# Kernel optimization log

Hardware: AMD Instinct MI355X
Metric: run time of the kernel (lower is better)

## Reference

```python
import jax, jax.numpy as jnp
import numpy as np

EMBED_DIM = 1024
NUM_HEADS = 16
HEAD_DIM = EMBED_DIM // NUM_HEADS


def setup_inputs() -> dict:
    key = jax.random.key(0)
    ks = jax.random.split(key, 11)
    B, S, E = 4, 2048, EMBED_DIM
    s = 1.0 / np.sqrt(E)
    return {
        "q": jax.random.normal(ks[0], (B, S, E), jnp.float32),
        "k": jax.random.normal(ks[1], (B, S, E), jnp.float32),
        "v": jax.random.normal(ks[2], (B, S, E), jnp.float32),
        "Wq": jax.random.uniform(ks[3], (E, E), jnp.float32, -s, s),
        "bq": jax.random.uniform(ks[4], (E,), jnp.float32, -s, s),
        "Wk": jax.random.uniform(ks[5], (E, E), jnp.float32, -s, s),
        "bk": jax.random.uniform(ks[6], (E,), jnp.float32, -s, s),
        "Wv": jax.random.uniform(ks[7], (E, E), jnp.float32, -s, s),
        "bv": jax.random.uniform(ks[8], (E,), jnp.float32, -s, s),
        "Wo": jax.random.uniform(ks[9], (E, E), jnp.float32, -s, s),
        "bo": jax.random.uniform(ks[10], (E,), jnp.float32, -s, s),
    }


def _split_heads(x):
    B, S, E = x.shape
    return x.reshape(B, S, NUM_HEADS, HEAD_DIM).transpose(0, 2, 1, 3)  # [B,H,S,D]


def reference(q, k, v, Wq, bq, Wk, bk, Wv, bv, Wo, bo):
    # torch Linear: x @ W.T + b
    Q = _split_heads(q @ Wq.T + bq)
    K = _split_heads(k @ Wk.T + bk)
    V = _split_heads(v @ Wv.T + bv)
    scale = 1.0 / jnp.sqrt(jnp.float32(HEAD_DIM))
    scores = jnp.einsum("bhqd,bhkd->bhqk", Q, K) * scale  # [B,H,S,S]
    weights = jax.nn.softmax(scores, axis=-1)
    ctx = jnp.einsum("bhqk,bhkd->bhqd", weights, V)
    B, H, S, D = ctx.shape
    merged = ctx.transpose(0, 2, 1, 3).reshape(B, S, H * D)
    out = merged @ Wo.T + bo
    return out, weights
```

## Files before the change

kernel.cpp:

```cpp
#include <hip/hip_runtime.h>
#include <hip/hip_bf16.h>

typedef __bf16 bf16x8 __attribute__((ext_vector_type(8)));
typedef float f32x4 __attribute__((ext_vector_type(4)));

constexpr size_t XQ_OFF = 0;
constexpr size_t WQ_OFF = 25165824;
constexpr size_t Q_OFF  = 29360128;
constexpr size_t KK_OFF = 37748736;
constexpr size_t VT_OFF = 46137344;
constexpr size_t CTX_OFF= 54525952;

__device__ __forceinline__ void gload16(const void* g, void* s) {
    __builtin_amdgcn_global_load_lds((__attribute__((address_space(1))) void*)g,
                                     (__attribute__((address_space(3))) void*)s, 16, 0, 0);
}
#define WAIT_VM0()   asm volatile("s_waitcnt vmcnt(0)" ::: "memory")
#define WAIT_VM4()   asm volatile("s_waitcnt vmcnt(4)" ::: "memory")
#define WAIT_LGKM0() asm volatile("s_waitcnt lgkmcnt(0)" ::: "memory")
#define BAR()        __builtin_amdgcn_s_barrier()

__global__ __launch_bounds__(256) void convert_k(
    const float* __restrict__ q, const float* __restrict__ k, const float* __restrict__ v,
    const float* __restrict__ Wq, const float* __restrict__ Wk, const float* __restrict__ Wv,
    const float* __restrict__ Wo, __bf16* __restrict__ ws) {
    int id = blockIdx.x * 256 + threadIdx.x;
    const int NX = 1048576;
    const int NW = 131072;
    const float* src; size_t dst; int local;
    if (id < 3 * NX) {
        int z = id / NX; local = id - z * NX;
        src = (z == 0) ? q : ((z == 1) ? k : v);
        dst = XQ_OFF + (size_t)z * 8388608;
    } else {
        int i2 = id - 3 * NX;
        int z = i2 / NW; local = i2 - z * NW;
        src = (z == 0) ? Wq : ((z == 1) ? Wk : ((z == 2) ? Wv : Wo));
        dst = WQ_OFF + (size_t)z * 1048576;
    }
    const float4* s4 = (const float4*)(src + (size_t)local * 8);
    float4 a = s4[0], b = s4[1];
    bf16x8 o;
    o[0]=(__bf16)a.x; o[1]=(__bf16)a.y; o[2]=(__bf16)a.z; o[3]=(__bf16)a.w;
    o[4]=(__bf16)b.x; o[5]=(__bf16)b.y; o[6]=(__bf16)b.z; o[7]=(__bf16)b.w;
    *(bf16x8*)(ws + dst + (size_t)local * 8) = o;
}

template<int MODE>
__global__ __launch_bounds__(256) void gemm_k(
    __bf16* __restrict__ ws,
    const float* __restrict__ bq, const float* __restrict__ bk,
    const float* __restrict__ bv, const float* __restrict__ bo,
    float* __restrict__ out) {
    const int K = 1024;
    unsigned n = blockIdx.x + 64u * (blockIdx.y + 8u * blockIdx.z);
    unsigned cpx = (MODE == 0) ? 192u : 64u;
    unsigned m_ = (n & 7u) * cpx + (n >> 3);
    unsigned bx = m_ & 63u;
    unsigned rest = m_ >> 6;
    unsigned by = rest & 7u;
    unsigned bz = rest >> 3;

    int z = (int)bz;
    const __bf16* A; const __bf16* Bm; const float* bias;
    if (MODE == 0) {
        A    = ws + XQ_OFF + (size_t)z * 8388608;
        Bm   = ws + WQ_OFF + (size_t)z * 1048576;
        bias = (z == 0) ? bq : ((z == 1) ? bk : bv);
    } else {
        A    = ws + CTX_OFF;
        Bm   = ws + WQ_OFF + (size_t)3 * 1048576;
        bias = bo;
    }
    int row0 = (int)bx * 128, col0 = (int)by * 128;
    __shared__ __align__(16) __bf16 As[2][128 * 32];
    __shared__ __align__(16) __bf16 Bs[2][128 * 32];
    int t = threadIdx.x, lane = t & 63, w = t >> 6;
    int wr = w >> 1, wc = w & 1;
    f32x4 acc[4][4];
#pragma unroll
    for (int i = 0; i < 4; ++i)
#pragma unroll
        for (int j = 0; j < 4; ++j) acc[i][j] = (f32x4){0.f, 0.f, 0.f, 0.f};

    auto stage = [&](int buf, int kt) {
#pragma unroll
        for (int i = 0; i < 2; ++i) {
            int e = ((i * 4 + w) * 64 + lane) * 8;
            int r = e >> 5, c = e & 31;
            gload16(A  + (size_t)(row0 + r) * K + kt + c, &As[buf][e]);
            gload16(Bm + (size_t)(col0 + r) * K + kt + c, &Bs[buf][e]);
        }
    };

    stage(0, 0);
    int cur = 0;
    for (int kt = 0; kt < K; kt += 32) {
        bool nx = kt + 32 < K;
        if (nx) { stage(cur ^ 1, kt + 32); WAIT_VM4(); }
        else    { WAIT_VM0(); }
        BAR();
        const __bf16* Ac = As[cur];
        const __bf16* Bc = Bs[cur];
        bf16x8 af[4], bfr[4];
#pragma unroll
        for (int f = 0; f < 4; ++f) {
            af[f]  = *(const bf16x8*)&Ac[(wr * 64 + f * 16 + (lane & 15)) * 32 + (lane >> 4) * 8];
            bfr[f] = *(const bf16x8*)&Bc[(wc * 64 + f * 16 + (lane & 15)) * 32 + (lane >> 4) * 8];
        }
#pragma unroll
        for (int fr = 0; fr < 4; ++fr)
#pragma unroll
            for (int fc = 0; fc < 4; ++fc)
                acc[fr][fc] = __builtin_amdgcn_mfma_f32_16x16x32_bf16(af[fr], bfr[fc], acc[fr][fc], 0, 0, 0);
        WAIT_LGKM0();
        BAR();
        cur ^= 1;
    }

    if (MODE == 0) {
        __bf16* dqk = ws + Q_OFF + (size_t)z * 8388608;
        __bf16* dvt = ws + VT_OFF;
#pragma unroll
        for (int fr = 0; fr < 4; ++fr)
#pragma unroll
            for (int fc = 0; fc < 4; ++fc)
#pragma unroll
                for (int r = 0; r < 4; ++r) {
                    int m = row0 + wr * 64 + fr * 16 + ((lane >> 4) << 2) + r;
                    int nn = col0 + wc * 64 + fc * 16 + (lane & 15);
                    float val = acc[fr][fc][r] + bias[nn];
                    int bb = m >> 11, s = m & 2047, h = nn >> 6, d = nn & 63;
                    size_t bh = (size_t)bb * 16 + h;
                    if (z < 2) dqk[bh * 131072 + (size_t)s * 64 + d] = (__bf16)val;
                    else       dvt[bh * 131072 + (size_t)d * 2048 + s] = (__bf16)val;
                }
    } else {
#pragma unroll
        for (int fr = 0; fr < 4; ++fr)
#pragma unroll
            for (int fc = 0; fc < 4; ++fc)
#pragma unroll
                for (int r = 0; r < 4; ++r) {
                    int m = row0 + wr * 64 + fr * 16 + ((lane >> 4) << 2) + r;
                    int nn = col0 + wc * 64 + fc * 16 + (lane & 15);
                    out[(size_t)m * 1024 + nn] = acc[fr][fc][r] + bias[nn];
                }
    }
}

__global__ __launch_bounds__(512) void attn_k(const __bf16* __restrict__ ws,
                                              __bf16* __restrict__ wsw,
                                              float* __restrict__ wout) {
    const __bf16* Qp  = ws + Q_OFF;
    const __bf16* Kp  = ws + KK_OFF;
    const __bf16* Vtp = ws + VT_OFF;
    __bf16* ctx = wsw + CTX_OFF;

    unsigned n = blockIdx.x + 16u * blockIdx.y;
    int bh = (int)((n & 7u) * 8u + ((n >> 3) >> 4));
    int q0 = (int)((n >> 3) & 15u) * 128;

    int t = threadIdx.x, lane = t & 63, w = t >> 6, g = lane >> 4;
    __shared__ __align__(16) __bf16 QP[128 * 64];
    __shared__ __align__(16) __bf16 Ks[2][64 * 64];
    __shared__ __align__(16) __bf16 Vts[2][64 * 64];
    const __bf16* Qb = Qp  + (size_t)bh * 131072;
    const __bf16* Kb = Kp  + (size_t)bh * 131072;
    const __bf16* Vb = Vtp + (size_t)bh * 131072;
    const float SCALE = 0.125f;

#pragma unroll
    for (int i = 0; i < 2; ++i) {
        int ch = t + 512 * i, r = ch >> 3, c8 = ch & 7;
        gload16(Qb + (size_t)(q0 + r) * 64 + ((c8 ^ (r & 7)) << 3), &QP[ch * 8]);
    }
    WAIT_VM0(); BAR();
    int qrow = w * 16 + (lane & 15);
    bf16x8 aq0 = *(const bf16x8*)((const char*)QP + qrow * 128 + ((g * 16) ^ ((qrow & 7) << 4)));
    bf16x8 aq1 = *(const bf16x8*)((const char*)QP + qrow * 128 + (((4 + g) * 16) ^ ((qrow & 7) << 4)));

    {
        int r = t >> 3, c8 = t & 7;
        gload16(Kb + (size_t)r * 64 + ((c8 ^ (r & 7)) << 3), &Ks[0][t * 8]);
    }
    WAIT_VM0(); BAR();
    float rs[4] = {0.f, 0.f, 0.f, 0.f};
    int cur = 0;
    for (int kt = 0; kt < 2048; kt += 64) {
        bool nx = kt < 1984;
        if (nx) {
            int r = t >> 3, c8 = t & 7;
            gload16(Kb + (size_t)(kt + 64 + r) * 64 + ((c8 ^ (r & 7)) << 3), &Ks[cur ^ 1][t * 8]);
        }
        const __bf16* Kc = Ks[cur];
#pragma unroll
        for (int kc = 0; kc < 4; ++kc) {
            int krow = kc * 16 + (lane & 15);
            bf16x8 b0 = *(const bf16x8*)((const char*)Kc + krow * 128 + ((g * 16) ^ ((krow & 7) << 4)));
            bf16x8 b1 = *(const bf16x8*)((const char*)Kc + krow * 128 + (((4 + g) * 16) ^ ((krow & 7) << 4)));
            f32x4 s = (f32x4){0.f, 0.f, 0.f, 0.f};
            s = __builtin_amdgcn_mfma_f32_16x16x32_bf16(aq0, b0, s, 0, 0, 0);
            s = __builtin_amdgcn_mfma_f32_16x16x32_bf16(aq1, b1, s, 0, 0, 0);
#pragma unroll
            for (int r4 = 0; r4 < 4; ++r4) rs[r4] += __expf(s[r4] * SCALE);
        }
        WAIT_LGKM0();
        if (nx) WAIT_VM0();
        BAR();
        cur ^= 1;
    }
#pragma unroll
    for (int m = 1; m < 16; m <<= 1)
#pragma unroll
        for (int r4 = 0; r4 < 4; ++r4) rs[r4] += __shfl_xor(rs[r4], m);
    float rinv[4];
#pragma unroll
    for (int r4 = 0; r4 < 4; ++r4) rinv[r4] = 1.f / rs[r4];

    {
        int r = t >> 3, c8 = t & 7;
        gload16(Kb + (size_t)r * 64   + ((c8 ^ (r & 7)) << 3), &Ks[0][t * 8]);
        gload16(Vb + (size_t)r * 2048 + ((c8 ^ (r & 7)) << 3), &Vts[0][t * 8]);
    }
    WAIT_VM0(); BAR();
    cur = 0;
    f32x4 cacc[4];
#pragma unroll
    for (int i = 0; i < 4; ++i) cacc[i] = (f32x4){0.f, 0.f, 0.f, 0.f};

    for (int kt = 0; kt < 2048; kt += 64) {
        bool nx = kt < 1984;
        if (nx) {
            int r = t >> 3, c8 = t & 7;
            gload16(Kb + (size_t)(kt + 64 + r) * 64 + ((c8 ^ (r & 7)) << 3), &Ks[cur ^ 1][t * 8]);
            gload16(Vb + (size_t)r * 2048 + (kt + 64) + ((c8 ^ (r & 7)) << 3), &Vts[cur ^ 1][t * 8]);
        }
        const __bf16* Kc = Ks[cur];
        const __bf16* Vc = Vts[cur];
#pragma unroll
        for (int kc = 0; kc < 4; ++kc) {
            int krow = kc * 16 + (lane & 15);
            bf16x8 b0 = *(const bf16x8*)((const char*)Kc + krow * 128 + ((g * 16) ^ ((krow & 7) << 4)));
            bf16x8 b1 = *(const bf16x8*)((const char*)Kc + krow * 128 + (((4 + g) * 16) ^ ((krow & 7) << 4)));
            f32x4 s = (f32x4){0.f, 0.f, 0.f, 0.f};
            s = __builtin_amdgcn_mfma_f32_16x16x32_bf16(aq0, b0, s, 0, 0, 0);
            s = __builtin_amdgcn_mfma_f32_16x16x32_bf16(aq1, b1, s, 0, 0, 0);
#pragma unroll
            for (int r4 = 0; r4 < 4; ++r4) {
                float e = __expf(s[r4] * SCALE) * rinv[r4];
                int prow = w * 16 + (g << 2) + r4;
                int pcol = kc * 16 + (lane & 15);
                *(__bf16*)((char*)QP + prow * 128 + ((pcol * 2) ^ ((prow & 7) << 4))) = (__bf16)e;
            }
        }
        WAIT_LGKM0();
        __builtin_amdgcn_sched_barrier(0);
        BAR();
#pragma unroll
        for (int i = 0; i < 2; ++i) {
            int ch = t + 512 * i, row = ch >> 3, c8 = ch & 7;
            bf16x8 p = *(const bf16x8*)((const char*)QP + row * 128 + ((c8 * 16) ^ ((row & 7) << 4)));
            f32x4 lo = (f32x4){(float)p[0], (float)p[1], (float)p[2], (float)p[3]};
            f32x4 hi = (f32x4){(float)p[4], (float)p[5], (float)p[6], (float)p[7]};
            float* dst = wout + ((size_t)bh * 2048 + q0 + row) * 2048 + kt + c8 * 8;
            *(f32x4*)dst = lo;
            *(f32x4*)(dst + 4) = hi;
        }
        int arow = w * 16 + (lane & 15);
#pragma unroll
        for (int ks = 0; ks < 2; ++ks) {
            bf16x8 ap = *(const bf16x8*)((const char*)QP + arow * 128 + ((ks * 64 + g * 16) ^ ((arow & 7) << 4)));
#pragma unroll
            for (int dc = 0; dc < 4; ++dc) {
                int vrow = dc * 16 + (lane & 15);
                bf16x8 bv = *(const bf16x8*)((const char*)Vc + vrow * 128 + ((ks * 64 + g * 16) ^ ((vrow & 7) << 4)));
                cacc[dc] = __builtin_amdgcn_mfma_f32_16x16x32_bf16(ap, bv, cacc[dc], 0, 0, 0);
            }
        }
        WAIT_LGKM0();
        if (nx) WAIT_VM0();
        BAR();
        cur ^= 1;
    }

    int bb = bh >> 4, h = bh & 15;
#pragma unroll
    for (int dc = 0; dc < 4; ++dc)
#pragma unroll
        for (int r4 = 0; r4 < 4; ++r4) {
            int qg = q0 + w * 16 + (g << 2) + r4;
            int d = dc * 16 + (lane & 15);
            ctx[((size_t)bb * 2048 + qg) * 1024 + h * 64 + d] = (__bf16)cacc[dc][r4];
        }
}

extern "C" void kernel_launch(void* const* d_in, const int* in_sizes, int n_in,
                              void* d_out, int out_size, void* d_ws, size_t ws_size,
                              hipStream_t stream) {
    const float* q  = (const float*)d_in[0];
    const float* k  = (const float*)d_in[1];
    const float* v  = (const float*)d_in[2];
    const float* Wq = (const float*)d_in[3];
    const float* bq = (const float*)d_in[4];
    const float* Wk = (const float*)d_in[5];
    const float* bk = (const float*)d_in[6];
    const float* Wv = (const float*)d_in[7];
    const float* bv = (const float*)d_in[8];
    const float* Wo = (const float*)d_in[9];
    const float* bo = (const float*)d_in[10];
    __bf16* ws = (__bf16*)d_ws;
    float* out  = (float*)d_out;
    float* wout = out + 8388608;

    convert_k<<<dim3(14336), dim3(256), 0, stream>>>(q, k, v, Wq, Wk, Wv, Wo, ws);
    gemm_k<0><<<dim3(64, 8, 3), dim3(256), 0, stream>>>(ws, bq, bk, bv, bo, out);
    attn_k<<<dim3(16, 64), dim3(512), 0, stream>>>(ws, ws, wout);
    gemm_k<1><<<dim3(64, 8, 1), dim3(256), 0, stream>>>(ws, bq, bk, bv, bo, out);
}
```

Before: 580.0 us.

## Split attention into rowsum and weights kernels with 256-row query tiles

The fused attention kernel is split into two launches. A rowsum kernel computes softmax denominators into workspace, and a weights/context kernel reads them. Each block now covers 256 query rows with two MFMA fragments per wave, which doubles reuse of each K/V tile loaded into LDS. The change also adds s_setprio around MFMA sections and relaxes the end-of-iteration wait to vmcnt(8) so weight-output stores need not drain. Costs are an extra launch, more LDS and registers per block, half as many blocks, and the rowsum buffer aliasing the start of the workspace where the converted q input sits (presumably dead by then).

```diff
diff --git a/kernel.cpp b/kernel.cpp
--- a/kernel.cpp
+++ b/kernel.cpp
@@ -17,6 +17,7 @@
 }
 #define WAIT_VM0()   asm volatile("s_waitcnt vmcnt(0)" ::: "memory")
 #define WAIT_VM4()   asm volatile("s_waitcnt vmcnt(4)" ::: "memory")
+#define WAIT_VM8()   asm volatile("s_waitcnt vmcnt(8)" ::: "memory")
 #define WAIT_LGKM0() asm volatile("s_waitcnt lgkmcnt(0)" ::: "memory")
 #define BAR()        __builtin_amdgcn_s_barrier()
 
@@ -149,43 +150,31 @@
     }
 }
 
-__global__ __launch_bounds__(512) void attn_k(const __bf16* __restrict__ ws,
-                                              __bf16* __restrict__ wsw,
-                                              float* __restrict__ wout) {
-    const __bf16* Qp  = ws + Q_OFF;
-    const __bf16* Kp  = ws + KK_OFF;
-    const __bf16* Vtp = ws + VT_OFF;
-    __bf16* ctx = wsw + CTX_OFF;
-
-    unsigned n = blockIdx.x + 16u * blockIdx.y;
-    int bh = (int)((n & 7u) * 8u + ((n >> 3) >> 4));
-    int q0 = (int)((n >> 3) & 15u) * 128;
-
+__global__ __launch_bounds__(512) void rowsum_k(const __bf16* __restrict__ ws,
+                                                float* __restrict__ rs_out) {
+    unsigned n = blockIdx.x + 8u * blockIdx.y;
+    unsigned m = (n & 7u) * 64u + (n >> 3);
+    int bh = (int)(m >> 3);
+    int q0 = (int)(m & 7u) * 256;
+    const __bf16* Qb = ws + Q_OFF  + (size_t)bh * 131072;
+    const __bf16* Kb = ws + KK_OFF + (size_t)bh * 131072;
+    __shared__ __align__(16) __bf16 Ks[2][64 * 64];
     int t = threadIdx.x, lane = t & 63, w = t >> 6, g = lane >> 4;
-    __shared__ __align__(16) __bf16 QP[128 * 64];
-    __shared__ __align__(16) __bf16 Ks[2][64 * 64];
-    __shared__ __align__(16) __bf16 Vts[2][64 * 64];
-    const __bf16* Qb = Qp  + (size_t)bh * 131072;
-    const __bf16* Kb = Kp  + (size_t)bh * 131072;
-    const __bf16* Vb = Vtp + (size_t)bh * 131072;
     const float SCALE = 0.125f;
 
-#pragma unroll
-    for (int i = 0; i < 2; ++i) {
-        int ch = t + 512 * i, r = ch >> 3, c8 = ch & 7;
-        gload16(Qb + (size_t)(q0 + r) * 64 + ((c8 ^ (r & 7)) << 3), &QP[ch * 8]);
-    }
+    bf16x8 aq[2][2];
+#pragma unroll
+    for (int f = 0; f < 2; ++f) {
+        int qr = q0 + w * 32 + f * 16 + (lane & 15);
+        aq[f][0] = *(const bf16x8*)&Qb[(size_t)qr * 64 + g * 8];
+        aq[f][1] = *(const bf16x8*)&Qb[(size_t)qr * 64 + 32 + g * 8];
+    }
+
+    { int r = t >> 3, c8 = t & 7;
+      gload16(Kb + (size_t)r * 64 + ((c8 ^ (r & 7)) << 3), &Ks[0][t * 8]); }
     WAIT_VM0(); BAR();
-    int qrow = w * 16 + (lane & 15);
-    bf16x8 aq0 = *(const bf16x8*)((const char*)QP + qrow * 128 + ((g * 16) ^ ((qrow & 7) << 4)));
-    bf16x8 aq1 = *(const bf16x8*)((const char*)QP + qrow * 128 + (((4 + g) * 16) ^ ((qrow & 7) << 4)));
-
-    {
-        int r = t >> 3, c8 = t & 7;
-        gload16(Kb + (size_t)r * 64 + ((c8 ^ (r & 7)) << 3), &Ks[0][t * 8]);
-    }
-    WAIT_VM0(); BAR();
-    float rs[4] = {0.f, 0.f, 0.f, 0.f};
+
+    float rs[8] = {0.f,0.f,0.f,0.f,0.f,0.f,0.f,0.f};
     int cur = 0;
     for (int kt = 0; kt < 2048; kt += 64) {
         bool nx = kt < 1984;
@@ -194,41 +183,94 @@
             gload16(Kb + (size_t)(kt + 64 + r) * 64 + ((c8 ^ (r & 7)) << 3), &Ks[cur ^ 1][t * 8]);
         }
         const __bf16* Kc = Ks[cur];
+        __builtin_amdgcn_s_setprio(1);
 #pragma unroll
         for (int kc = 0; kc < 4; ++kc) {
             int krow = kc * 16 + (lane & 15);
             bf16x8 b0 = *(const bf16x8*)((const char*)Kc + krow * 128 + ((g * 16) ^ ((krow & 7) << 4)));
             bf16x8 b1 = *(const bf16x8*)((const char*)Kc + krow * 128 + (((4 + g) * 16) ^ ((krow & 7) << 4)));
-            f32x4 s = (f32x4){0.f, 0.f, 0.f, 0.f};
-            s = __builtin_amdgcn_mfma_f32_16x16x32_bf16(aq0, b0, s, 0, 0, 0);
-            s = __builtin_amdgcn_mfma_f32_16x16x32_bf16(aq1, b1, s, 0, 0, 0);
-#pragma unroll
-            for (int r4 = 0; r4 < 4; ++r4) rs[r4] += __expf(s[r4] * SCALE);
-        }
+#pragma unroll
+            for (int f = 0; f < 2; ++f) {
+                f32x4 s = (f32x4){0.f, 0.f, 0.f, 0.f};
+                s = __builtin_amdgcn_mfma_f32_16x16x32_bf16(aq[f][0], b0, s, 0, 0, 0);
+                s = __builtin_amdgcn_mfma_f32_16x16x32_bf16(aq[f][1], b1, s, 0, 0, 0);
+#pragma unroll
+                for (int r4 = 0; r4 < 4; ++r4) rs[f * 4 + r4] += __expf(s[r4] * SCALE);
+            }
+        }
+        __builtin_amdgcn_s_setprio(0);
         WAIT_LGKM0();
         if (nx) WAIT_VM0();
         BAR();
         cur ^= 1;
     }
 #pragma unroll
-    for (int m = 1; m < 16; m <<= 1)
-#pragma unroll
-        for (int r4 = 0; r4 < 4; ++r4) rs[r4] += __shfl_xor(rs[r4], m);
-    float rinv[4];
-#pragma unroll
-    for (int r4 = 0; r4 < 4; ++r4) rinv[r4] = 1.f / rs[r4];
-
-    {
-        int r = t >> 3, c8 = t & 7;
-        gload16(Kb + (size_t)r * 64   + ((c8 ^ (r & 7)) << 3), &Ks[0][t * 8]);
-        gload16(Vb + (size_t)r * 2048 + ((c8 ^ (r & 7)) << 3), &Vts[0][t * 8]);
+    for (int msk = 1; msk < 16; msk <<= 1)
+#pragma unroll
+        for (int i = 0; i < 8; ++i) rs[i] += __shfl_xor(rs[i], msk);
+    if ((lane & 15) == 0) {
+#pragma unroll
+        for (int f = 0; f < 2; ++f)
+#pragma unroll
+            for (int r4 = 0; r4 < 4; ++r4)
+                rs_out[(size_t)bh * 2048 + q0 + w * 32 + f * 16 + g * 4 + r4] = rs[f * 4 + r4];
+    }
+}
+
+__global__ __launch_bounds__(512) void attnw_k(const __bf16* __restrict__ ws,
+                                               const float* __restrict__ rsf,
+                                               __bf16* __restrict__ wsw,
+                                               float* __restrict__ wout) {
+    unsigned n = blockIdx.x + 8u * blockIdx.y;
+    unsigned m = (n & 7u) * 64u + (n >> 3);
+    int bh = (int)(m >> 3);
+    int q0 = (int)(m & 7u) * 256;
+
+    const __bf16* Qb = ws + Q_OFF  + (size_t)bh * 131072;
+    const __bf16* Kb = ws + KK_OFF + (size_t)bh * 131072;
+    const __bf16* Vb = ws + VT_OFF + (size_t)bh * 131072;
+    __bf16* ctx = wsw + CTX_OFF;
+
+    int t = threadIdx.x, lane = t & 63, w = t >> 6, g = lane >> 4;
+    __shared__ __align__(16) __bf16 QP[256 * 64];
+    __shared__ __align__(16) __bf16 Ks[2][64 * 64];
+    __shared__ __align__(16) __bf16 Vts[2][64 * 64];
+    const float SCALE = 0.125f;
+
+    float rinv[8];
+#pragma unroll
+    for (int f = 0; f < 2; ++f)
+#pragma unroll
+        for (int r4 = 0; r4 < 4; ++r4)
+            rinv[f * 4 + r4] = 1.f / rsf[(size_t)bh * 2048 + q0 + w * 32 + f * 16 + g * 4 + r4];
+
+#pragma unroll
+    for (int i = 0; i < 4; ++i) {
+        int ch = t + 512 * i, r = ch >> 3, c8 = ch & 7;
+        gload16(Qb + (size_t)(q0 + r) * 64 + ((c8 ^ (r & 7)) << 3), &QP[ch * 8]);
     }
     WAIT_VM0(); BAR();
-    cur = 0;
-    f32x4 cacc[4];
-#pragma unroll
-    for (int i = 0; i < 4; ++i) cacc[i] = (f32x4){0.f, 0.f, 0.f, 0.f};
-
+    bf16x8 aq[2][2];
+#pragma unroll
+    for (int f = 0; f < 2; ++f) {
+        int qrow = w * 32 + f * 16 + (lane & 15);
+        aq[f][0] = *(const bf16x8*)((const char*)QP + qrow * 128 + ((g * 16) ^ ((qrow & 7) << 4)));
+        aq[f][1] = *(const bf16x8*)((const char*)QP + qrow * 128 + (((4 + g) * 16) ^ ((qrow & 7) << 4)));
+    }
+    WAIT_LGKM0(); BAR();
+
+    { int r = t >> 3, c8 = t & 7;
+      gload16(Kb + (size_t)r * 64   + ((c8 ^ (r & 7)) << 3), &Ks[0][t * 8]);
+      gload16(Vb + (size_t)r * 2048 + ((c8 ^ (r & 7)) << 3), &Vts[0][t * 8]); }
+    WAIT_VM0(); BAR();
+
+    f32x4 cacc[2][4];
+#pragma unroll
+    for (int f = 0; f < 2; ++f)
+#pragma unroll
+        for (int dc = 0; dc < 4; ++dc) cacc[f][dc] = (f32x4){0.f, 0.f, 0.f, 0.f};
+
+    int cur = 0;
     for (int kt = 0; kt < 2048; kt += 64) {
         bool nx = kt < 1984;
         if (nx) {
@@ -238,27 +280,32 @@
         }
         const __bf16* Kc = Ks[cur];
         const __bf16* Vc = Vts[cur];
+        __builtin_amdgcn_s_setprio(1);
 #pragma unroll
         for (int kc = 0; kc < 4; ++kc) {
             int krow = kc * 16 + (lane & 15);
             bf16x8 b0 = *(const bf16x8*)((const char*)Kc + krow * 128 + ((g * 16) ^ ((krow & 7) << 4)));
             bf16x8 b1 = *(const bf16x8*)((const char*)Kc + krow * 128 + (((4 + g) * 16) ^ ((krow & 7) << 4)));
-            f32x4 s = (f32x4){0.f, 0.f, 0.f, 0.f};
-            s = __builtin_amdgcn_mfma_f32_16x16x32_bf16(aq0, b0, s, 0, 0, 0);
-            s = __builtin_amdgcn_mfma_f32_16x16x32_bf16(aq1, b1, s, 0, 0, 0);
-#pragma unroll
-            for (int r4 = 0; r4 < 4; ++r4) {
-                float e = __expf(s[r4] * SCALE) * rinv[r4];
-                int prow = w * 16 + (g << 2) + r4;
-                int pcol = kc * 16 + (lane & 15);
-                *(__bf16*)((char*)QP + prow * 128 + ((pcol * 2) ^ ((prow & 7) << 4))) = (__bf16)e;
-            }
-        }
+#pragma unroll
+            for (int f = 0; f < 2; ++f) {
+                f32x4 s = (f32x4){0.f, 0.f, 0.f, 0.f};
+                s = __builtin_amdgcn_mfma_f32_16x16x32_bf16(aq[f][0], b0, s, 0, 0, 0);
+                s = __builtin_amdgcn_mfma_f32_16x16x32_bf16(aq[f][1], b1, s, 0, 0, 0);
+#pragma unroll
+                for (int r4 = 0; r4 < 4; ++r4) {
+                    float e = __expf(s[r4] * SCALE) * rinv[f * 4 + r4];
+                    int prow = w * 32 + f * 16 + (g << 2) + r4;
+                    int pcol = kc * 16 + (lane & 15);
+                    *(__bf16*)((char*)QP + prow * 128 + ((pcol * 2) ^ ((prow & 7) << 4))) = (__bf16)e;
+                }
+            }
+        }
+        __builtin_amdgcn_s_setprio(0);
         WAIT_LGKM0();
         __builtin_amdgcn_sched_barrier(0);
         BAR();
 #pragma unroll
-        for (int i = 0; i < 2; ++i) {
+        for (int i = 0; i < 4; ++i) {
             int ch = t + 512 * i, row = ch >> 3, c8 = ch & 7;
             bf16x8 p = *(const bf16x8*)((const char*)QP + row * 128 + ((c8 * 16) ^ ((row & 7) << 4)));
             f32x4 lo = (f32x4){(float)p[0], (float)p[1], (float)p[2], (float)p[3]};
@@ -267,32 +314,42 @@
             *(f32x4*)dst = lo;
             *(f32x4*)(dst + 4) = hi;
         }
-        int arow = w * 16 + (lane & 15);
+        __builtin_amdgcn_s_setprio(1);
 #pragma unroll
         for (int ks = 0; ks < 2; ++ks) {
-            bf16x8 ap = *(const bf16x8*)((const char*)QP + arow * 128 + ((ks * 64 + g * 16) ^ ((arow & 7) << 4)));
+            bf16x8 ap[2];
+#pragma unroll
+            for (int f = 0; f < 2; ++f) {
+                int arow = w * 32 + f * 16 + (lane & 15);
+                ap[f] = *(const bf16x8*)((const char*)QP + arow * 128 + ((ks * 64 + g * 16) ^ ((arow & 7) << 4)));
+            }
 #pragma unroll
             for (int dc = 0; dc < 4; ++dc) {
                 int vrow = dc * 16 + (lane & 15);
                 bf16x8 bv = *(const bf16x8*)((const char*)Vc + vrow * 128 + ((ks * 64 + g * 16) ^ ((vrow & 7) << 4)));
-                cacc[dc] = __builtin_amdgcn_mfma_f32_16x16x32_bf16(ap, bv, cacc[dc], 0, 0, 0);
-            }
-        }
+#pragma unroll
+                for (int f = 0; f < 2; ++f)
+                    cacc[f][dc] = __builtin_amdgcn_mfma_f32_16x16x32_bf16(ap[f], bv, cacc[f][dc], 0, 0, 0);
+            }
+        }
+        __builtin_amdgcn_s_setprio(0);
         WAIT_LGKM0();
-        if (nx) WAIT_VM0();
+        WAIT_VM8();
         BAR();
         cur ^= 1;
     }
 
     int bb = bh >> 4, h = bh & 15;
 #pragma unroll
-    for (int dc = 0; dc < 4; ++dc)
-#pragma unroll
-        for (int r4 = 0; r4 < 4; ++r4) {
-            int qg = q0 + w * 16 + (g << 2) + r4;
-            int d = dc * 16 + (lane & 15);
-            ctx[((size_t)bb * 2048 + qg) * 1024 + h * 64 + d] = (__bf16)cacc[dc][r4];
-        }
+    for (int f = 0; f < 2; ++f)
+#pragma unroll
+        for (int dc = 0; dc < 4; ++dc)
+#pragma unroll
+            for (int r4 = 0; r4 < 4; ++r4) {
+                int qg = q0 + w * 32 + f * 16 + (g << 2) + r4;
+                int d = dc * 16 + (lane & 15);
+                ctx[((size_t)bb * 2048 + qg) * 1024 + h * 64 + d] = (__bf16)cacc[f][dc][r4];
+            }
 }
 
 extern "C" void kernel_launch(void* const* d_in, const int* in_sizes, int n_in,
@@ -312,9 +369,11 @@
     __bf16* ws = (__bf16*)d_ws;
     float* out  = (float*)d_out;
     float* wout = out + 8388608;
+    float* rsum = (float*)d_ws;
 
     convert_k<<<dim3(14336), dim3(256), 0, stream>>>(q, k, v, Wq, Wk, Wv, Wo, ws);
     gemm_k<0><<<dim3(64, 8, 3), dim3(256), 0, stream>>>(ws, bq, bk, bv, bo, out);
-    attn_k<<<dim3(16, 64), dim3(512), 0, stream>>>(ws, ws, wout);
+    rowsum_k<<<dim3(8, 64), dim3(512), 0, stream>>>(ws, rsum);
+    attnw_k<<<dim3(8, 64), dim3(512), 0, stream>>>(ws, rsum, ws, wout);
     gemm_k<1><<<dim3(64, 8, 1), dim3(256), 0, stream>>>(ws, bq, bk, bv, bo, out);
 }
```

Result: faster. 542.4 us (-6.5%).
